# Performance work log

Measured on AMD Instinct MI355X. Metric: run time of the kernel, lower is better.

Reference implementation:

```python
import jax, jax.numpy as jnp
from jax import lax
import numpy as np


def setup_inputs() -> dict:
    key = jax.random.key(0)
    ks = jax.random.split(key, 7)
    B, T, F, H, O = 4096, 256, 18, 64, 15
    s = 1.0 / np.sqrt(H)  # PyTorch uniform(-1/sqrt(H), 1/sqrt(H)) init scale
    return {
        "X": jax.random.normal(ks[0], (B, T, F), dtype=jnp.float32),
        "W_ih": jax.random.uniform(ks[1], (4 * H, F), jnp.float32, -s, s),
        "W_hh": jax.random.uniform(ks[2], (4 * H, H), jnp.float32, -s, s),
        "b_ih": jax.random.uniform(ks[3], (4 * H,), jnp.float32, -s, s),
        "b_hh": jax.random.uniform(ks[4], (4 * H,), jnp.float32, -s, s),
        "W_cls": jax.random.uniform(ks[5], (O, H), jnp.float32, -s, s),
        "b_cls": jax.random.uniform(ks[6], (O,), jnp.float32, -s, s),
    }


def _lstm_last_h(X, W_ih, W_hh, b_ih, b_hh):
    # X: [B, T, F]; PyTorch gate order in the 4H axis: i, f, g, o
    B = X.shape[0]
    H = W_hh.shape[1]
    # Input contribution for all timesteps at once: [B, T, 4H]
    xg = jnp.einsum("btf,gf->btg", X, W_ih) + b_ih + b_hh
    xg_t = jnp.swapaxes(xg, 0, 1)  # [T, B, 4H] for scan over time

    def step(carry, xg_step):
        h, c = carry
        gates = xg_step + h @ W_hh.T  # [B, 4H]
        i, f, g, o = jnp.split(gates, 4, axis=-1)
        i = jax.nn.sigmoid(i)
        f = jax.nn.sigmoid(f)
        g = jnp.tanh(g)
        o = jax.nn.sigmoid(o)
        c = f * c + i * g
        h = o * jnp.tanh(c)
        return (h, c), None

    h0 = jnp.zeros((B, H), dtype=X.dtype)
    c0 = jnp.zeros((B, H), dtype=X.dtype)
    (h, c), _ = lax.scan(step, (h0, c0), xg_t)
    return h  # last-timestep hidden state, [B, H]


def reference(X, W_ih, W_hh, b_ih, b_hh, W_cls, b_cls):
    h_last = _lstm_last_h(X, W_ih, W_hh, b_ih, b_hh)
    out = h_last @ W_cls.T + b_cls  # [B, n_outputs]
    return out
```

## Files before the change

### kernel.cpp

```cpp
#include <hip/hip_runtime.h>
#include <hip/hip_bf16.h>

typedef __attribute__((ext_vector_type(8))) __bf16 bf16x8;
typedef __attribute__((ext_vector_type(4))) float  f32x4;

#define T_SEQ 256
#define F_IN  18
#define HID   64
#define NB    16
#define NO    15

static __device__ __forceinline__ float rcp_fast(float x) {
    return __builtin_amdgcn_rcpf(x);
}
static __device__ __forceinline__ float sigm(float x) {
    return rcp_fast(1.0f + __expf(-x));
}
static __device__ __forceinline__ float tanh_fast(float x) {
    return 1.0f - 2.0f * rcp_fast(__expf(2.0f * x) + 1.0f);
}

#define BARRIER_LDS() asm volatile("s_waitcnt lgkmcnt(0)\n\ts_barrier" ::: "memory")

__global__ __launch_bounds__(1024, 4) void lstm_fused(
    const float* __restrict__ X,
    const float* __restrict__ Wih,
    const float* __restrict__ Whh,
    const float* __restrict__ bih,
    const float* __restrict__ bhh,
    const float* __restrict__ Wcls,
    const float* __restrict__ bcls,
    float* __restrict__ out)
{
    const int tid = threadIdx.x;
    const int l   = tid & 63;
    const int w   = tid >> 6;
    const int q   = l >> 4;
    const int bb  = l & 15;
    const int b0  = blockIdx.x * NB;

    __shared__ __align__(16) __bf16 hbuf[2][8][NB][8];
    __shared__ __align__(16) __bf16 xbuf[2][8][NB][8];
    __shared__ float h32[NB][HID];

    const int sb = (tid >> 3) & 15;
    const int sk = ((tid >> 7) << 3) | (tid & 7);
    int f_s, part_s;
    if (sk < 18)      { f_s = sk;      part_s = 0; }
    else if (sk < 36) { f_s = sk - 18; part_s = 0; }
    else if (sk < 54) { f_s = sk - 36; part_s = 1; }
    else              { f_s = 0;       part_s = 2; }
    const float* xsrc = X + ((long)(b0 + sb) * T_SEQ) * F_IN + f_s;
    __bf16* const xbase = &xbuf[0][0][0][0];

    {
        __bf16* hz = &hbuf[0][0][0][0];
        for (int i = tid; i < 8 * NB * 8; i += 1024) hz[i] = (__bf16)0.0f;
    }
    {
        const float v = (part_s == 2) ? 0.0f : xsrc[0];
        const __bf16 hi = (__bf16)v;
        xbase[tid] = (part_s == 1) ? (__bf16)(v - (float)hi) : hi;
    }
    float xq[4];
#pragma unroll
    for (int i = 0; i < 4; ++i)
        xq[i] = (part_s == 2) ? 0.0f : xsrc[(1 + i) * F_IN];

    bf16x8 whh_hi[2], whh_lo[2], wih[2];
    {
        const int prow = 16 * w + bb;
        const int jrow = (prow & 3) * 64 + (prow >> 2);
#pragma unroll
        for (int kk = 0; kk < 2; ++kk) {
            bf16x8 hi, lo, xa;
#pragma unroll
            for (int r = 0; r < 8; ++r) {
                const int k = 32 * kk + 8 * q + r;
                const float v = Whh[jrow * HID + k];
                const __bf16 vh = (__bf16)v;
                hi[r] = vh;
                lo[r] = (__bf16)(v - (float)vh);
                int f, part;
                if (k < 18)      { f = k;      part = 0; }
                else if (k < 36) { f = k - 18; part = 1; }
                else if (k < 54) { f = k - 36; part = 0; }
                else             { f = 0;      part = 2; }
                const float wv = (part == 2) ? 0.0f : Wih[jrow * F_IN + f];
                const __bf16 wh = (__bf16)wv;
                xa[r] = (part == 1) ? (__bf16)(wv - (float)wh) : wh;
            }
            whh_hi[kk] = hi;
            whh_lo[kk] = lo;
            wih[kk]    = xa;
        }
    }

    const int u_c = 4 * w + q;
    float bias4[4];
#pragma unroll
    for (int r = 0; r < 4; ++r) bias4[r] = bih[r * 64 + u_c] + bhh[r * 64 + u_c];

    __bf16* const hw_base = &hbuf[0][0][0][0] +
                            ((u_c >> 3) * 128 + bb * 8 + (u_c & 7));
    const __bf16* const hr_base = &hbuf[0][0][0][0] + 8 * (size_t)l;
    const __bf16* const xr_base = &xbuf[0][0][0][0] + 8 * (size_t)l;

    __syncthreads();

    float cst = 0.0f;

#define STEP(t_, PF, LAST)                                                          \
    {                                                                               \
        const int cur_ = (t_) & 1;                                                  \
        const int nxt_ = cur_ ^ 1;                                                  \
        const int s_   = (t_) & 3;                                                  \
        const __bf16* hr = hr_base + cur_ * 1024;                                   \
        const __bf16* xr = xr_base + cur_ * 1024;                                   \
        const bf16x8 bx0 = *reinterpret_cast<const bf16x8*>(xr);                    \
        const bf16x8 bx1 = *reinterpret_cast<const bf16x8*>(xr + 512);              \
        const bf16x8 bh0 = *reinterpret_cast<const bf16x8*>(hr);                    \
        const bf16x8 bh1 = *reinterpret_cast<const bf16x8*>(hr + 512);              \
        {                                                                           \
            const float vs = xq[s_];                                                \
            const __bf16 sh = (__bf16)vs;                                           \
            xbase[nxt_ * 1024 + tid] = (part_s == 1) ? (__bf16)(vs - (float)sh) : sh; \
        }                                                                           \
        {                                                                           \
            const int tl_ = PF ? (((t_) + 5 < T_SEQ) ? (t_) + 5 : (T_SEQ - 1))      \
                               : ((t_) + 5);                                        \
            xq[s_] = (part_s == 2) ? 0.0f : xsrc[tl_ * F_IN];                       \
        }                                                                           \
        __builtin_amdgcn_s_setprio(1);                                              \
        f32x4 acc_a = {bias4[0], bias4[1], bias4[2], bias4[3]};                     \
        f32x4 acc_b = {0.0f, 0.0f, 0.0f, 0.0f};                                     \
        f32x4 acc_c = {0.0f, 0.0f, 0.0f, 0.0f};                                     \
        acc_a = __builtin_amdgcn_mfma_f32_16x16x32_bf16(wih[0],    bx0, acc_a, 0, 0, 0); \
        acc_b = __builtin_amdgcn_mfma_f32_16x16x32_bf16(wih[1],    bx1, acc_b, 0, 0, 0); \
        acc_c = __builtin_amdgcn_mfma_f32_16x16x32_bf16(whh_lo[0], bh0, acc_c, 0, 0, 0); \
        acc_a = __builtin_amdgcn_mfma_f32_16x16x32_bf16(whh_hi[0], bh0, acc_a, 0, 0, 0); \
        acc_b = __builtin_amdgcn_mfma_f32_16x16x32_bf16(whh_hi[1], bh1, acc_b, 0, 0, 0); \
        acc_c = __builtin_amdgcn_mfma_f32_16x16x32_bf16(whh_lo[1], bh1, acc_c, 0, 0, 0); \
        const f32x4 acc = (acc_a + acc_b) + acc_c;                                  \
        const float gi = sigm(acc[0]);                                              \
        const float gf = sigm(acc[1]);                                              \
        const float gg = tanh_fast(acc[2]);                                         \
        const float go = sigm(acc[3]);                                              \
        const float c  = gf * cst + gi * gg;                                        \
        cst = c;                                                                    \
        const float h  = go * tanh_fast(c);                                         \
        hw_base[nxt_ * 1024] = (__bf16)h;                                           \
        __builtin_amdgcn_s_setprio(0);                                              \
        if (LAST) h32[bb][u_c] = h;                                                 \
        BARRIER_LDS();                                                              \
    }

#pragma unroll 4
    for (int t = 0; t < 248; ++t) {
        STEP(t, 0, 0)
    }
#pragma unroll
    for (int tt = 248; tt < T_SEQ; ++tt) {
        STEP(tt, 1, (tt == T_SEQ - 1))
    }
#undef STEP

    if (tid < NB * NO) {
        const int bo = tid / NO;
        const int o  = tid % NO;
        float ssum = bcls[o];
#pragma unroll 8
        for (int k = 0; k < HID; ++k)
            ssum += h32[bo][k] * Wcls[o * HID + k];
        out[(long)(b0 + bo) * NO + o] = ssum;
    }
}

extern "C" void kernel_launch(void* const* d_in, const int* in_sizes, int n_in,
                              void* d_out, int out_size, void* d_ws, size_t ws_size,
                              hipStream_t stream)
{
    const float* X    = (const float*)d_in[0];
    const float* Wih  = (const float*)d_in[1];
    const float* Whh  = (const float*)d_in[2];
    const float* bih  = (const float*)d_in[3];
    const float* bhh  = (const float*)d_in[4];
    const float* Wcls = (const float*)d_in[5];
    const float* bcls = (const float*)d_in[6];
    float* outp = (float*)d_out;

    dim3 grid(4096 / NB);
    dim3 block(1024);
    lstm_fused<<<grid, block, 0, stream>>>(X, Wih, Whh, bih, bhh, Wcls, bcls, outp);
}
```

Baseline: 254.7 us.

## Merge x and h operands into one K-concatenated buffer, drop W_hh lo split

Concatenates the input features (with a hi/lo split of W_ih applied only on the weight side) and the hidden state into a single 128-wide K vector in one shared buffer. This cuts the recurrent matmul from six MFMAs over three accumulator chains to four MFMAs over two. The low-order bf16 correction for W_hh is dropped, and only a subset of threads stage x. The cost is lower precision in the recurrent weights, which may increase numerical error over 256 timesteps.

```diff
diff --git a/kernel.cpp b/kernel.cpp
--- a/kernel.cpp
+++ b/kernel.cpp
@@ -39,60 +39,48 @@
     const int bb  = l & 15;
     const int b0  = blockIdx.x * NB;
 
-    __shared__ __align__(16) __bf16 hbuf[2][8][NB][8];
-    __shared__ __align__(16) __bf16 xbuf[2][8][NB][8];
+    __shared__ __align__(16) __bf16 ubuf[2][16][NB][8];
     __shared__ float h32[NB][HID];
 
+    const int sk = ((tid >> 7) << 3) | (tid & 7);
     const int sb = (tid >> 3) & 15;
-    const int sk = ((tid >> 7) << 3) | (tid & 7);
-    int f_s, part_s;
-    if (sk < 18)      { f_s = sk;      part_s = 0; }
-    else if (sk < 36) { f_s = sk - 18; part_s = 0; }
-    else if (sk < 54) { f_s = sk - 36; part_s = 1; }
-    else              { f_s = 0;       part_s = 2; }
+    const bool stager = (tid < 640) && (sk < 36);
+    const int f_s = (sk < 18) ? sk : (sk - 18);
     const float* xsrc = X + ((long)(b0 + sb) * T_SEQ) * F_IN + f_s;
-    __bf16* const xbase = &xbuf[0][0][0][0];
+    __bf16* const ubase = &ubuf[0][0][0][0];
 
-    {
-        __bf16* hz = &hbuf[0][0][0][0];
-        for (int i = tid; i < 8 * NB * 8; i += 1024) hz[i] = (__bf16)0.0f;
-    }
-    {
-        const float v = (part_s == 2) ? 0.0f : xsrc[0];
-        const __bf16 hi = (__bf16)v;
-        xbase[tid] = (part_s == 1) ? (__bf16)(v - (float)hi) : hi;
-    }
+    for (int i = tid; i < 2 * 16 * NB * 8; i += 1024) ubase[i] = (__bf16)0.0f;
+
+    if (stager) ubase[tid] = (__bf16)xsrc[0];
     float xq[4];
 #pragma unroll
     for (int i = 0; i < 4; ++i)
-        xq[i] = (part_s == 2) ? 0.0f : xsrc[(1 + i) * F_IN];
+        xq[i] = stager ? xsrc[(1 + i) * F_IN] : 0.0f;
 
-    bf16x8 whh_hi[2], whh_lo[2], wih[2];
+    bf16x8 afrag[4];
     {
         const int prow = 16 * w + bb;
         const int jrow = (prow & 3) * 64 + (prow >> 2);
 #pragma unroll
-        for (int kk = 0; kk < 2; ++kk) {
-            bf16x8 hi, lo, xa;
+        for (int j = 0; j < 4; ++j) {
+            bf16x8 v;
 #pragma unroll
             for (int r = 0; r < 8; ++r) {
-                const int k = 32 * kk + 8 * q + r;
-                const float v = Whh[jrow * HID + k];
-                const __bf16 vh = (__bf16)v;
-                hi[r] = vh;
-                lo[r] = (__bf16)(v - (float)vh);
-                int f, part;
-                if (k < 18)      { f = k;      part = 0; }
-                else if (k < 36) { f = k - 18; part = 1; }
-                else if (k < 54) { f = k - 36; part = 0; }
-                else             { f = 0;      part = 2; }
-                const float wv = (part == 2) ? 0.0f : Wih[jrow * F_IN + f];
-                const __bf16 wh = (__bf16)wv;
-                xa[r] = (part == 1) ? (__bf16)(wv - (float)wh) : wh;
+                const int k = 32 * j + 8 * q + r;
+                float val;
+                if (k < 18) {
+                    val = Wih[jrow * F_IN + k];
+                } else if (k < 36) {
+                    const float wv = Wih[jrow * F_IN + (k - 18)];
+                    val = wv - (float)((__bf16)wv);
+                } else if (k < 100) {
+                    val = Whh[jrow * HID + (k - 36)];
+                } else {
+                    val = 0.0f;
+                }
+                v[r] = (__bf16)val;
             }
-            whh_hi[kk] = hi;
-            whh_lo[kk] = lo;
-            wih[kk]    = xa;
+            afrag[j] = v;
         }
     }
 
@@ -101,10 +89,9 @@
 #pragma unroll
     for (int r = 0; r < 4; ++r) bias4[r] = bih[r * 64 + u_c] + bhh[r * 64 + u_c];
 
-    __bf16* const hw_base = &hbuf[0][0][0][0] +
-                            ((u_c >> 3) * 128 + bb * 8 + (u_c & 7));
-    const __bf16* const hr_base = &hbuf[0][0][0][0] + 8 * (size_t)l;
-    const __bf16* const xr_base = &xbuf[0][0][0][0] + 8 * (size_t)l;
+    const int hslot = 36 + u_c;
+    __bf16* const hw_base = ubase + ((hslot >> 3) * 128 + bb * 8 + (hslot & 7));
+    const __bf16* const rd_base = ubase + 8 * (size_t)l;
 
     __syncthreads();
 
@@ -115,33 +102,25 @@
         const int cur_ = (t_) & 1;                                                  \
         const int nxt_ = cur_ ^ 1;                                                  \
         const int s_   = (t_) & 3;                                                  \
-        const __bf16* hr = hr_base + cur_ * 1024;                                   \
-        const __bf16* xr = xr_base + cur_ * 1024;                                   \
-        const bf16x8 bx0 = *reinterpret_cast<const bf16x8*>(xr);                    \
-        const bf16x8 bx1 = *reinterpret_cast<const bf16x8*>(xr + 512);              \
-        const bf16x8 bh0 = *reinterpret_cast<const bf16x8*>(hr);                    \
-        const bf16x8 bh1 = *reinterpret_cast<const bf16x8*>(hr + 512);              \
-        {                                                                           \
-            const float vs = xq[s_];                                                \
-            const __bf16 sh = (__bf16)vs;                                           \
-            xbase[nxt_ * 1024 + tid] = (part_s == 1) ? (__bf16)(vs - (float)sh) : sh; \
-        }                                                                           \
-        {                                                                           \
+        const __bf16* rp = rd_base + cur_ * 2048;                                   \
+        const bf16x8 bf0 = *reinterpret_cast<const bf16x8*>(rp);                    \
+        const bf16x8 bf1 = *reinterpret_cast<const bf16x8*>(rp + 512);              \
+        const bf16x8 bf2 = *reinterpret_cast<const bf16x8*>(rp + 1024);             \
+        const bf16x8 bf3 = *reinterpret_cast<const bf16x8*>(rp + 1536);             \
+        if (stager) {                                                               \
+            ubase[nxt_ * 2048 + tid] = (__bf16)xq[s_];                              \
             const int tl_ = PF ? (((t_) + 5 < T_SEQ) ? (t_) + 5 : (T_SEQ - 1))      \
                                : ((t_) + 5);                                        \
-            xq[s_] = (part_s == 2) ? 0.0f : xsrc[tl_ * F_IN];                       \
+            xq[s_] = xsrc[tl_ * F_IN];                                              \
         }                                                                           \
         __builtin_amdgcn_s_setprio(1);                                              \
         f32x4 acc_a = {bias4[0], bias4[1], bias4[2], bias4[3]};                     \
         f32x4 acc_b = {0.0f, 0.0f, 0.0f, 0.0f};                                     \
-        f32x4 acc_c = {0.0f, 0.0f, 0.0f, 0.0f};                                     \
-        acc_a = __builtin_amdgcn_mfma_f32_16x16x32_bf16(wih[0],    bx0, acc_a, 0, 0, 0); \
-        acc_b = __builtin_amdgcn_mfma_f32_16x16x32_bf16(wih[1],    bx1, acc_b, 0, 0, 0); \
-        acc_c = __builtin_amdgcn_mfma_f32_16x16x32_bf16(whh_lo[0], bh0, acc_c, 0, 0, 0); \
-        acc_a = __builtin_amdgcn_mfma_f32_16x16x32_bf16(whh_hi[0], bh0, acc_a, 0, 0, 0); \
-        acc_b = __builtin_amdgcn_mfma_f32_16x16x32_bf16(whh_hi[1], bh1, acc_b, 0, 0, 0); \
-        acc_c = __builtin_amdgcn_mfma_f32_16x16x32_bf16(whh_lo[1], bh1, acc_c, 0, 0, 0); \
-        const f32x4 acc = (acc_a + acc_b) + acc_c;                                  \
+        acc_a = __builtin_amdgcn_mfma_f32_16x16x32_bf16(afrag[0], bf0, acc_a, 0, 0, 0); \
+        acc_b = __builtin_amdgcn_mfma_f32_16x16x32_bf16(afrag[1], bf1, acc_b, 0, 0, 0); \
+        acc_a = __builtin_amdgcn_mfma_f32_16x16x32_bf16(afrag[2], bf2, acc_a, 0, 0, 0); \
+        acc_b = __builtin_amdgcn_mfma_f32_16x16x32_bf16(afrag[3], bf3, acc_b, 0, 0, 0); \
+        const f32x4 acc = acc_a + acc_b;                                            \
         const float gi = sigm(acc[0]);                                              \
         const float gf = sigm(acc[1]);                                              \
         const float gg = tanh_fast(acc[2]);                                         \
@@ -149,7 +128,7 @@
         const float c  = gf * cst + gi * gg;                                        \
         cst = c;                                                                    \
         const float h  = go * tanh_fast(c);                                         \
-        hw_base[nxt_ * 1024] = (__bf16)h;                                           \
+        hw_base[nxt_ * 2048] = (__bf16)h;                                           \
         __builtin_amdgcn_s_setprio(0);                                              \
         if (LAST) h32[bb][u_c] = h;                                                 \
         BARRIER_LDS();                                                              \
```

New measurement: 233.6 us. 8.3% less time.
